# Optimization experiments

Hardware: AMD Instinct MI355X
Metric: run time of the kernel (lower is better)

Reference implementation:

```python
import math
import jax, jax.numpy as jnp
import numpy as np

N_HEAD = 8
BLOCK_SIZE = 1024
LN_EPS = 1e-5


def _layer_norm(x, g, b):
    mu = jnp.mean(x, axis=-1, keepdims=True)
    var = jnp.var(x, axis=-1, keepdims=True)
    return (x - mu) * jax.lax.rsqrt(var + LN_EPS) * g + b


def _skew(QEr):
    # QEr: (B, nh, L, L) -> pad one zero column on the left, reshape, drop first row
    B, nh, nr, nc = QEr.shape
    padded = jnp.pad(QEr, ((0, 0), (0, 0), (0, 0), (1, 0)))  # (B, nh, nr, nc+1)
    reshaped = padded.reshape(B, nh, nc + 1, nr)
    return reshaped[:, :, 1:, :]  # (B, nh, nr, nc)


def _attn(x, W_qkv, b_qkv, W_o, b_o, Er):
    B, L, D = x.shape
    hs = D // N_HEAD
    qkv = x @ W_qkv + b_qkv  # (B, L, 3D)
    q, k, v = jnp.split(qkv, 3, axis=-1)
    # (B, nh, L, hs)
    q = q.reshape(B, L, N_HEAD, hs).transpose(0, 2, 1, 3)
    k = k.reshape(B, L, N_HEAD, hs).transpose(0, 2, 1, 3)
    v = v.reshape(B, L, N_HEAD, hs).transpose(0, 2, 1, 3)
    start = BLOCK_SIZE - L
    Er_t = Er[start:, :].T  # (hs, L)
    QEr = q @ Er_t  # (B, nh, L, L)
    Srel = _skew(QEr)
    scores = (jnp.einsum('bhqd,bhkd->bhqk', q, k) + Srel) * (1.0 / math.sqrt(hs))
    causal = jnp.tril(jnp.ones((L, L), dtype=bool))
    scores = jnp.where(causal, scores, jnp.float32(-jnp.inf))
    att = jax.nn.softmax(scores, axis=-1)
    y = jnp.einsum('bhqk,bhkd->bhqd', att, v)
    y = y.transpose(0, 2, 1, 3).reshape(B, L, D)
    return y @ W_o + b_o


def reference(x, W_qkv, b_qkv, W_o, b_o, Er, ln1_g, ln1_b, ln2_g, ln2_b,
              W_fc, b_fc, W_proj, b_proj):
    x = x + _attn(_layer_norm(x, ln1_g, ln1_b), W_qkv, b_qkv, W_o, b_o, Er)
    h = _layer_norm(x, ln2_g, ln2_b) @ W_fc + b_fc
    h = jax.nn.gelu(h, approximate=False)
    h = h @ W_proj + b_proj
    return x + h


def setup_inputs() -> dict:
    key = jax.random.key(0)
    ks = jax.random.split(key, 8)
    B, L, D, F = 8, 1024, 1024, 4096
    hs = D // N_HEAD
    s = lambda fan_in: 1.0 / math.sqrt(fan_in)
    return {
        'x': jax.random.normal(ks[0], (B, L, D), dtype=jnp.float32),
        'W_qkv': jax.random.normal(ks[1], (D, 3 * D), dtype=jnp.float32) * s(D),
        'b_qkv': jnp.zeros((3 * D,), dtype=jnp.float32),
        'W_o': jax.random.normal(ks[2], (D, D), dtype=jnp.float32) * s(D),
        'b_o': jnp.zeros((D,), dtype=jnp.float32),
        'Er': jax.random.normal(ks[3], (BLOCK_SIZE, hs), dtype=jnp.float32),
        'ln1_g': jnp.ones((D,), dtype=jnp.float32),
        'ln1_b': jnp.zeros((D,), dtype=jnp.float32),
        'ln2_g': jnp.ones((D,), dtype=jnp.float32),
        'ln2_b': jnp.zeros((D,), dtype=jnp.float32),
        'W_fc': jax.random.normal(ks[4], (D, F), dtype=jnp.float32) * s(D),
        'b_fc': jnp.zeros((F,), dtype=jnp.float32),
        'W_proj': jax.random.normal(ks[5], (F, D), dtype=jnp.float32) * s(F),
        'b_proj': jnp.zeros((D,), dtype=jnp.float32),
    }
```

## Files before the change

kernel.cpp:

```cpp
#include <hip/hip_runtime.h>
#include <hip/hip_bf16.h>
#include <math.h>

#define BB 8
#define LL 1024
#define DD 1024
#define FF 4096
#define NHH 8
#define HSS 128
#define SCALE 0.08838834764831845f
#define TRI(qi, kt) ((qi) * ((qi) + 1) / 2 + (kt))

typedef __bf16 bf16;
typedef __bf16 bf16x8 __attribute__((ext_vector_type(8)));
typedef float f32x4 __attribute__((ext_vector_type(4)));
typedef _Float16 f16;
typedef _Float16 f16x4 __attribute__((ext_vector_type(4)));

__device__ inline void async_copy16(const void* g, void* l) {
  __builtin_amdgcn_global_load_lds(
      (const __attribute__((address_space(1))) unsigned int*)g,
      (__attribute__((address_space(3))) unsigned int*)l, 16, 0, 0);
}

#define FENCE() asm volatile("" ::: "memory")
#define BARRIER() do { FENCE(); __builtin_amdgcn_s_barrier(); FENCE(); } while (0)
#define VMCNT0() asm volatile("s_waitcnt vmcnt(0)" ::: "memory")
#define VMCNT2() asm volatile("s_waitcnt vmcnt(2)" ::: "memory")
#define VMCNT4() asm volatile("s_waitcnt vmcnt(4)" ::: "memory")
#define VMCNT6() asm volatile("s_waitcnt vmcnt(6)" ::: "memory")

__global__ __launch_bounds__(256)
void transpose_cast_kernel(const float* __restrict__ W, bf16* __restrict__ Wt,
                           int K, int N) {
  __shared__ float tile[32][33];
  int n0 = blockIdx.x * 32, k0 = blockIdx.y * 32;
  int tx = threadIdx.x, ty = threadIdx.y;
#pragma unroll
  for (int i = 0; i < 32; i += 8)
    tile[ty + i][tx] = W[(size_t)(k0 + ty + i) * N + n0 + tx];
  __syncthreads();
#pragma unroll
  for (int i = 0; i < 32; i += 8)
    Wt[(size_t)(n0 + ty + i) * K + k0 + tx] = (bf16)tile[tx][ty + i];
}

__global__ __launch_bounds__(256)
void pack_er_kernel(const float* __restrict__ Er, bf16* __restrict__ ErP) {
  int g = blockIdx.x, tid = threadIdx.x;
  int l15 = tid & 15, quad = (tid >> 4) & 3, st = tid >> 6;
  const float* src = Er + (size_t)(g * 16 + l15) * HSS + st * 32 + quad * 8;
  bf16* dst = ErP + (size_t)g * 2048 + tid * 8;
#pragma unroll
  for (int j = 0; j < 8; j++) dst[j] = (bf16)src[j];
}

__global__ __launch_bounds__(256)
void ln_kernel(const float* __restrict__ x, const float* __restrict__ g,
               const float* __restrict__ bta, bf16* __restrict__ out) {
  int row = blockIdx.x;
  int tid = threadIdx.x;
  const float4 v = ((const float4*)(x + (size_t)row * DD))[tid];
  float s = v.x + v.y + v.z + v.w;
  float s2 = v.x * v.x + v.y * v.y + v.z * v.z + v.w * v.w;
#pragma unroll
  for (int o = 32; o > 0; o >>= 1) {
    s += __shfl_down(s, o);
    s2 += __shfl_down(s2, o);
  }
  __shared__ float a1[4], a2[4];
  int wave = tid >> 6;
  if ((tid & 63) == 0) { a1[wave] = s; a2[wave] = s2; }
  __syncthreads();
  s = a1[0] + a1[1] + a1[2] + a1[3];
  s2 = a2[0] + a2[1] + a2[2] + a2[3];
  float mu = s * (1.0f / DD);
  float rstd = rsqrtf(s2 * (1.0f / DD) - mu * mu + 1e-5f);
  float4 gv = ((const float4*)g)[tid];
  float4 bv = ((const float4*)bta)[tid];
  bf16* o4 = out + (size_t)row * DD + tid * 4;
  o4[0] = (bf16)((v.x - mu) * rstd * gv.x + bv.x);
  o4[1] = (bf16)((v.y - mu) * rstd * gv.y + bv.y);
  o4[2] = (bf16)((v.z - mu) * rstd * gv.z + bv.z);
  o4[3] = (bf16)((v.w - mu) * rstd * gv.w + bv.w);
}

template <int EPI>
__global__ __launch_bounds__(512)
void gemm256_kernel(const bf16* __restrict__ A, const bf16* __restrict__ Bt,
                    const float* __restrict__ bias, void* __restrict__ Cout,
                    int M, int N, int K) {
  __shared__ bf16 Als[2][256 * 64];
  __shared__ bf16 Bls[2][256 * 64];
  int tid = threadIdx.x;
  int wave = tid >> 6, lane = tid & 63;
  int l15 = lane & 15, quad = lane >> 4;
  int wmi = wave >> 2, wni = wave & 3;
  int m0 = blockIdx.y * 256, n0 = blockIdx.x * 256;

  int u0 = tid, u1 = tid + 512;
  int r0 = u0 >> 3, c0 = ((u0 & 7) ^ (r0 & 7)) << 3;
  int r1 = u1 >> 3, c1 = ((u1 & 7) ^ (r1 & 7)) << 3;
  const bf16* aB0 = A + (size_t)(m0 + r0) * K + c0;
  const bf16* aB1 = A + (size_t)(m0 + r1) * K + c1;
  const bf16* bB0 = Bt + (size_t)(n0 + r0) * K + c0;
  const bf16* bB1 = Bt + (size_t)(n0 + r1) * K + c1;
  int d0 = u0 * 8, d1 = u1 * 8;

  auto stageA = [&](int b, int h, int t) {
    size_t off = (size_t)h * 128 * K + (size_t)t * 64;
    async_copy16(aB0 + off, &Als[b][h * 8192 + d0]);
    async_copy16(aB1 + off, &Als[b][h * 8192 + d1]);
  };
  auto stageB = [&](int b, int h, int t) {
    size_t off = (size_t)h * 128 * K + (size_t)t * 64;
    async_copy16(bB0 + off, &Bls[b][h * 8192 + d0]);
    async_copy16(bB1 + off, &Bls[b][h * 8192 + d1]);
  };

  f32x4 acc[8][4] = {};
  bf16x8 af[2][4], bfr[2][2][2];

  auto readA = [&](int b, int qm) {
#pragma unroll
    for (int kk = 0; kk < 2; kk++)
#pragma unroll
      for (int mt = 0; mt < 4; mt++) {
        int ra = qm * 128 + wmi * 64 + mt * 16 + l15;
        af[kk][mt] = *(const bf16x8*)&Als[b][ra * 64 + (((kk * 4 + quad) ^ (ra & 7)) << 3)];
      }
  };
  auto readB = [&](int b, int qn) {
#pragma unroll
    for (int kk = 0; kk < 2; kk++)
#pragma unroll
      for (int nt = 0; nt < 2; nt++) {
        int rb = qn * 128 + wni * 32 + nt * 16 + l15;
        bfr[qn][kk][nt] = *(const bf16x8*)&Bls[b][rb * 64 + (((kk * 4 + quad) ^ (rb & 7)) << 3)];
      }
  };
  auto mfma16 = [&](int qm, int qn) {
    __builtin_amdgcn_s_setprio(1);
#pragma unroll
    for (int kk = 0; kk < 2; kk++)
#pragma unroll
      for (int mt = 0; mt < 4; mt++)
#pragma unroll
        for (int nt = 0; nt < 2; nt++)
          acc[qm * 4 + mt][qn * 2 + nt] = __builtin_amdgcn_mfma_f32_16x16x32_bf16(
              af[kk][mt], bfr[qn][kk][nt], acc[qm * 4 + mt][qn * 2 + nt], 0, 0, 0);
    __builtin_amdgcn_s_setprio(0);
  };

  int nk = K >> 6;
  stageA(0, 0, 0); stageB(0, 0, 0); stageB(0, 1, 0); stageA(0, 1, 0);
  stageA(1, 0, 1); stageB(1, 1, 1);
  VMCNT6();
  BARRIER();

  for (int t = 0; t < nk; t += 2) {
#pragma unroll
    for (int uu = 0; uu < 2; uu++) {
      const int tt = t + uu;
      const int cur = uu;
      readA(cur, 0); readB(cur, 0); readB(cur, 1);
      if (tt + 1 < nk) stageB(cur ^ 1, 0, tt + 1);
      BARRIER();
      mfma16(0, 0);
      BARRIER();
      if (tt + 1 < nk) stageA(cur ^ 1, 1, tt + 1);
      VMCNT6();
      BARRIER();
      mfma16(0, 1);
      BARRIER();
      readA(cur, 1);
      if (tt + 2 < nk) stageA(cur, 0, tt + 2);
      BARRIER();
      mfma16(1, 1);
      BARRIER();
      if (tt + 2 < nk) stageB(cur, 1, tt + 2);
      VMCNT6();
      BARRIER();
      mfma16(1, 0);
      BARRIER();
    }
  }

#pragma unroll
  for (int MT = 0; MT < 8; MT++) {
#pragma unroll
    for (int NT = 0; NT < 4; NT++) {
      int col = n0 + (NT >> 1) * 128 + wni * 32 + (NT & 1) * 16 + l15;
      float bv = bias[col];
#pragma unroll
      for (int r = 0; r < 4; r++) {
        int row = m0 + (MT >> 2) * 128 + wmi * 64 + (MT & 3) * 16 + quad * 4 + r;
        float v = acc[MT][NT][r] + bv;
        if (EPI == 1) v = 0.5f * v * (1.0f + erff(v * 0.7071067811865475f));
        ((bf16*)Cout)[(size_t)row * N + col] = (bf16)v;
      }
    }
  }
}

template <int EPI>
__global__ __launch_bounds__(512)
void gemm256n_kernel(const bf16* __restrict__ A, const bf16* __restrict__ Bt,
                     const float* __restrict__ bias, const float* __restrict__ res,
                     void* __restrict__ Cout, int M, int N, int K) {
  __shared__ bf16 Als[2][256 * 64];
  __shared__ bf16 Bls[2][128 * 64];
  int tid = threadIdx.x;
  int wave = tid >> 6, lane = tid & 63;
  int l15 = lane & 15, quad = lane >> 4;
  int wmi = wave >> 2, wni = wave & 3;
  int m0 = blockIdx.y * 256, n0 = blockIdx.x * 128;

  int u0 = tid, u1 = tid + 512;
  int r0 = u0 >> 3, c0 = ((u0 & 7) ^ (r0 & 7)) << 3;
  int r1 = u1 >> 3, c1 = ((u1 & 7) ^ (r1 & 7)) << 3;
  const bf16* aB0 = A + (size_t)(m0 + r0) * K + c0;
  const bf16* aB1 = A + (size_t)(m0 + r1) * K + c1;
  const bf16* bB0 = Bt + (size_t)(n0 + r0) * K + c0;
  const bf16* bB1 = Bt + (size_t)(n0 + r1) * K + c1;
  int d0 = u0 * 8, d1 = u1 * 8;

  auto stageA = [&](int b, int h, int t) {
    size_t off = (size_t)h * 128 * K + (size_t)t * 64;
    async_copy16(aB0 + off, &Als[b][h * 8192 + d0]);
    async_copy16(aB1 + off, &Als[b][h * 8192 + d1]);
  };
  auto stageB = [&](int b, int t) {
    size_t off = (size_t)t * 64;
    async_copy16(bB0 + off, &Bls[b][d0]);
    async_copy16(bB1 + off, &Bls[b][d1]);
  };

  f32x4 acc[8][2] = {};
  bf16x8 af[2][4], bfr[2][2];

  auto readA = [&](int b, int qm) {
#pragma unroll
    for (int kk = 0; kk < 2; kk++)
#pragma unroll
      for (int mt = 0; mt < 4; mt++) {
        int ra = qm * 128 + wmi * 64 + mt * 16 + l15;
        af[kk][mt] = *(const bf16x8*)&Als[b][ra * 64 + (((kk * 4 + quad) ^ (ra & 7)) << 3)];
      }
  };
  auto readB = [&](int b) {
#pragma unroll
    for (int kk = 0; kk < 2; kk++)
#pragma unroll
      for (int nt = 0; nt < 2; nt++) {
        int rb = wni * 32 + nt * 16 + l15;
        bfr[kk][nt] = *(const bf16x8*)&Bls[b][rb * 64 + (((kk * 4 + quad) ^ (rb & 7)) << 3)];
      }
  };
  auto mfma16 = [&](int qm) {
    __builtin_amdgcn_s_setprio(1);
#pragma unroll
    for (int kk = 0; kk < 2; kk++)
#pragma unroll
      for (int mt = 0; mt < 4; mt++)
#pragma unroll
        for (int nt = 0; nt < 2; nt++)
          acc[qm * 4 + mt][nt] = __builtin_amdgcn_mfma_f32_16x16x32_bf16(
              af[kk][mt], bfr[kk][nt], acc[qm * 4 + mt][nt], 0, 0, 0);
    __builtin_amdgcn_s_setprio(0);
  };

  int nk = K >> 6;
  stageB(0, 0); stageB(1, 1); stageA(0, 0, 0); stageA(0, 1, 0);
  VMCNT0();
  BARRIER();

  for (int t = 0; t < nk; t += 2) {
#pragma unroll
    for (int uu = 0; uu < 2; uu++) {
      const int tt = t + uu;
      const int cur = uu;
      readA(cur, 0); readB(cur);
      if (tt + 1 < nk) { stageA(cur ^ 1, 0, tt + 1); VMCNT4(); }
      else { VMCNT0(); }
      BARRIER();
      mfma16(0);
      BARRIER();
      readA(cur, 1);
      if (tt + 1 < nk) stageA(cur ^ 1, 1, tt + 1);
      if (tt + 2 < nk) { stageB(cur, tt + 2); VMCNT4(); }
      else { VMCNT2(); }
      BARRIER();
      mfma16(1);
      BARRIER();
    }
  }

#pragma unroll
  for (int MT = 0; MT < 8; MT++) {
#pragma unroll
    for (int NT = 0; NT < 2; NT++) {
      int col = n0 + wni * 32 + NT * 16 + l15;
      float bv = bias[col];
#pragma unroll
      for (int r = 0; r < 4; r++) {
        int row = m0 + (MT >> 2) * 128 + wmi * 64 + (MT & 3) * 16 + quad * 4 + r;
        float v = acc[MT][NT][r] + bv;
        if (EPI == 2) {
          v += res[(size_t)row * N + col];
          ((float*)Cout)[(size_t)row * N + col] = v;
        } else {
          ((bf16*)Cout)[(size_t)row * N + col] = (bf16)v;
        }
      }
    }
  }
}

template <int EPI>
__global__ __launch_bounds__(256)
void gemm_kernel(const bf16* __restrict__ A, const bf16* __restrict__ Bt,
                 const float* __restrict__ bias, const float* __restrict__ res,
                 void* __restrict__ Cout, int M, int N, int K) {
  __shared__ bf16 Als[128 * 64];
  __shared__ bf16 Bls[128 * 64];
  int tid = threadIdx.x;
  int wave = tid >> 6, lane = tid & 63;
  int l15 = lane & 15, quad = lane >> 4;

  int m0 = blockIdx.y * 128, n0 = blockIdx.x * 128;
  int wm = (wave >> 1) * 64, wn = (wave & 1) * 64;
  f32x4 acc[4][4] = {};

  const bf16* asrc[4];
  const bf16* bsrc[4];
  int ldso[4];
#pragma unroll
  for (int i = 0; i < 4; i++) {
    int u = i * 256 + tid;
    int row = u >> 3, c = u & 7;
    int g = c ^ (row & 7);
    asrc[i] = A + (size_t)(m0 + row) * K + g * 8;
    bsrc[i] = Bt + (size_t)(n0 + row) * K + g * 8;
    ldso[i] = u * 8;
  }

  for (int k0 = 0; k0 < K; k0 += 64) {
    __syncthreads();
#pragma unroll
    for (int i = 0; i < 4; i++) {
      async_copy16(asrc[i] + k0, &Als[ldso[i]]);
      async_copy16(bsrc[i] + k0, &Bls[ldso[i]]);
    }
    __syncthreads();

    bf16x8 af[2][4], bfr[2][4];
#pragma unroll
    for (int kk = 0; kk < 2; kk++) {
#pragma unroll
      for (int mt = 0; mt < 4; mt++) {
        int ra = wm + mt * 16 + l15;
        af[kk][mt] = *(const bf16x8*)&Als[ra * 64 + (((kk * 4 + quad) ^ (ra & 7)) << 3)];
        int rb = wn + mt * 16 + l15;
        bfr[kk][mt] = *(const bf16x8*)&Bls[rb * 64 + (((kk * 4 + quad) ^ (rb & 7)) << 3)];
      }
    }
#pragma unroll
    for (int kk = 0; kk < 2; kk++)
#pragma unroll
      for (int mt = 0; mt < 4; mt++)
#pragma unroll
        for (int nt = 0; nt < 4; nt++)
          acc[mt][nt] = __builtin_amdgcn_mfma_f32_16x16x32_bf16(af[kk][mt], bfr[kk][nt],
                                                                acc[mt][nt], 0, 0, 0);
  }

#pragma unroll
  for (int mt = 0; mt < 4; mt++) {
#pragma unroll
    for (int nt = 0; nt < 4; nt++) {
      int col = n0 + wn + nt * 16 + l15;
      float bv = bias[col];
#pragma unroll
      for (int r = 0; r < 4; r++) {
        int row = m0 + wm + mt * 16 + quad * 4 + r;
        float v = acc[mt][nt][r] + bv;
        if (EPI == 1) v = 0.5f * v * (1.0f + erff(v * 0.7071067811865475f));
        if (EPI == 2) {
          v += res[(size_t)row * N + col];
          ((float*)Cout)[(size_t)row * N + col] = v;
        } else {
          ((bf16*)Cout)[(size_t)row * N + col] = (bf16)v;
        }
      }
    }
  }
}

__global__ __launch_bounds__(256)
void pack_kv_kernel(const bf16* __restrict__ qkv, bf16* __restrict__ Kpack,
                    bf16* __restrict__ Vpack) {
  __shared__ bf16 Vst[64][132];
  int kt = blockIdx.x, h = blockIdx.y, b = blockIdx.z;
  int tid = threadIdx.x;
  const size_t rs = 3 * DD;
  const bf16* kb = qkv + (size_t)b * LL * rs + (size_t)(kt * 64) * rs + DD + h * HSS;
  const bf16* vb = kb + DD;
  bf16* kp = Kpack + ((size_t)(b * NHH + h) * 16 + kt) * (64 * 128);
  bf16* vp = Vpack + ((size_t)(b * NHH + h) * 16 + kt) * (128 * 64);
#pragma unroll
  for (int i = 0; i < 4; i++) {
    int u = i * 256 + tid;
    int kk = u >> 4, c = u & 15;
    bf16x8 kv = *(const bf16x8*)(kb + (size_t)kk * rs + c * 8);
    *(bf16x8*)(kp + kk * 128 + ((c ^ kk) & 15) * 8) = kv;
    *(bf16x8*)&Vst[kk][c * 8] = *(const bf16x8*)(vb + (size_t)kk * rs + c * 8);
  }
  __syncthreads();
#pragma unroll
  for (int i = 0; i < 4; i++) {
    int u = i * 256 + tid;
    int d = u >> 3, c = u & 7;
    bf16x8 t;
#pragma unroll
    for (int j = 0; j < 8; j++) t[j] = Vst[c * 8 + j][d];
    *(bf16x8*)(vp + d * 64 + ((c ^ (d & 7))) * 8) = t;
  }
}

__global__ __launch_bounds__(256)
void relband_kernel(const bf16* __restrict__ qkv, const bf16* __restrict__ ErP,
                    f16* __restrict__ band) {
  int tid = threadIdx.x, wave = tid >> 6, lane = tid & 63;
  int l15 = lane & 15, quad = lane >> 4;
  int h = blockIdx.y, b = blockIdx.z;
  const size_t rs = 3 * DD;
  const bf16* qbase = qkv + (size_t)b * LL * rs + h * HSS;
  f16* bbase = band + (size_t)(b * NHH + h) * (136 * 4096);

#pragma unroll 1
  for (int ph = 0; ph < 2; ph++) {
    int qb = ph ? 15 - blockIdx.x : blockIdx.x;
    int qw0 = qb * 64 + wave * 16;

    bf16x8 qf[4];
#pragma unroll
    for (int st = 0; st < 4; st++)
      qf[st] = *(const bf16x8*)(qbase + (size_t)(qw0 + l15) * rs + st * 32 + quad * 8);

#pragma unroll 1
    for (int kt = 0; kt <= qb; kt++) {
      int k0 = kt * 64;
      int kmax_off = qw0 + 15 - k0;
      int m_base = 1008 - qw0 + k0;
      int gb = m_base >> 4;
      int ntR = (kmax_off >> 4) + 1;
      if (ntR > 4) ntR = 4;

      f32x4 rr[5] = {};
#pragma unroll
      for (int n = 0; n < 5; n++) {
        if (n <= ntR) {
          int g = gb + n;
          if (g > 63) g = 63;
          const bf16* ep = ErP + (size_t)g * 2048 + lane * 8;
#pragma unroll
          for (int st = 0; st < 4; st++) {
            bf16x8 ef = *(const bf16x8*)(ep + st * 512);
            rr[n] = __builtin_amdgcn_mfma_f32_16x16x32_bf16(qf[st], ef, rr[n], 0, 0, 0);
          }
        }
      }

      f16x4 sf[4];
#pragma unroll
      for (int rg = 0; rg < 4; rg++) {
        int qloc = quad * 4 + rg;
        int tt = 15 - qloc + l15;
        int src = (lane & 48) | (tt & 15);
        float shv[5];
#pragma unroll
        for (int n = 0; n < 5; n++)
          shv[n] = (n <= ntR) ? __shfl(rr[n][rg], src) : 0.f;
#pragma unroll
        for (int nt = 0; nt < 4; nt++)
          sf[nt][rg] = (f16)((tt & 16) ? shv[nt + 1] : shv[nt]);
      }
      f16* tb = bbase + (size_t)TRI(qb, kt) * 4096;
#pragma unroll
      for (int nt = 0; nt < 4; nt++)
        if (nt * 16 <= kmax_off)
          *(f16x4*)(tb + (wave * 4 + nt) * 256 + l15 * 16 + quad * 4) = sf[nt];
    }
  }
}

__global__ __launch_bounds__(256)
void flash_kernel(const bf16* __restrict__ qkv, const bf16* __restrict__ Kpack,
                  const bf16* __restrict__ Vpack, const f16* __restrict__ band,
                  bf16* __restrict__ y) {
  __shared__ bf16 Kls[2][64 * 128];
  __shared__ bf16 Vls[2][128 * 64];
  __shared__ bf16 Pls[4][16][72];

  int tid = threadIdx.x, wave = tid >> 6, lane = tid & 63;
  int l15 = lane & 15, quad = lane >> 4;
  int h = blockIdx.y, b = blockIdx.z;

  const size_t rs = 3 * DD;
  const bf16* qbase = qkv + (size_t)b * LL * rs + h * HSS;
  const bf16* kp = Kpack + (size_t)(b * NHH + h) * 16 * (64 * 128);
  const bf16* vp = Vpack + (size_t)(b * NHH + h) * 16 * (128 * 64);
  const f16* bnd = band + (size_t)(b * NHH + h) * (136 * 4096);

  int buf = 0;
#pragma unroll 1
  for (int ph = 0; ph < 2; ph++) {
    int qb = ph ? 15 - blockIdx.x : blockIdx.x;
    int qw0 = qb * 64 + wave * 16;
    int nkt = qb + 1;

    bf16x8 qf[4];
#pragma unroll
    for (int st = 0; st < 4; st++)
      qf[st] = *(const bf16x8*)(qbase + (size_t)(qw0 + l15) * rs + st * 32 + quad * 8);

    {
      const bf16* ks = kp;
      const bf16* vs = vp;
#pragma unroll
      for (int i = 0; i < 4; i++) {
        int off = (wave * 4 + i) * 512 + lane * 8;
        async_copy16(ks + off, &Kls[buf][off]);
        async_copy16(vs + off, &Vls[buf][off]);
      }
    }

    f32x4 o[8] = {};
    float mrow[4] = {-INFINITY, -INFINITY, -INFINITY, -INFINITY};
    float lrow[4] = {0.f, 0.f, 0.f, 0.f};

#pragma unroll 1
    for (int kt = 0; kt < nkt; kt++) {
      int k0 = kt * 64;
      int kmax_off = qw0 + 15 - k0;
      __syncthreads();

      const f16* tb = bnd + (size_t)TRI(qb, kt) * 4096;
      f16x4 srl[4] = {};
#pragma unroll
      for (int nt = 0; nt < 4; nt++)
        if (nt * 16 <= kmax_off)
          srl[nt] = *(const f16x4*)(tb + (wave * 4 + nt) * 256 + l15 * 16 + quad * 4);

      if (kt + 1 < nkt) {
        const bf16* ks = kp + (size_t)(kt + 1) * (64 * 128);
        const bf16* vs = vp + (size_t)(kt + 1) * (128 * 64);
#pragma unroll
        for (int i = 0; i < 4; i++) {
          int off = (wave * 4 + i) * 512 + lane * 8;
          async_copy16(ks + off, &Kls[buf ^ 1][off]);
          async_copy16(vs + off, &Vls[buf ^ 1][off]);
        }
      }

      f32x4 sa[4] = {};
#pragma unroll
      for (int nt = 0; nt < 4; nt++) {
        if (nt * 16 <= kmax_off) {
          int kk = nt * 16 + l15;
#pragma unroll
          for (int st = 0; st < 4; st++) {
            bf16x8 kf = *(const bf16x8*)&Kls[buf][kk * 128 + (((st * 4 + quad) ^ l15) & 15) * 8];
            sa[nt] = __builtin_amdgcn_mfma_f32_16x16x32_bf16(qf[st], kf, sa[nt], 0, 0, 0);
          }
        }
      }

      float pmx[4] = {-INFINITY, -INFINITY, -INFINITY, -INFINITY};
#pragma unroll
      for (int nt = 0; nt < 4; nt++) {
        if (nt * 16 <= kmax_off) {
          int kg = k0 + nt * 16 + l15;
#pragma unroll
          for (int rg = 0; rg < 4; rg++) {
            int qg = qw0 + quad * 4 + rg;
            float v = (sa[nt][rg] + (float)srl[nt][rg]) * SCALE;
            v = (kg <= qg) ? v : -INFINITY;
            sa[nt][rg] = v;
            pmx[rg] = fmaxf(pmx[rg], v);
          }
        } else {
#pragma unroll
          for (int rg = 0; rg < 4; rg++) sa[nt][rg] = -INFINITY;
        }
      }

#pragma unroll
      for (int rg = 0; rg < 4; rg++) {
        float v = pmx[rg];
        v = fmaxf(v, __shfl_xor(v, 1));
        v = fmaxf(v, __shfl_xor(v, 2));
        v = fmaxf(v, __shfl_xor(v, 4));
        v = fmaxf(v, __shfl_xor(v, 8));
        float mnew = fmaxf(mrow[rg], v);
        float alpha = __expf(mrow[rg] - mnew);
        mrow[rg] = mnew;
        lrow[rg] *= alpha;
#pragma unroll
        for (int nt = 0; nt < 8; nt++) o[nt][rg] *= alpha;
        pmx[rg] = mnew;
      }
      float ls[4] = {0.f, 0.f, 0.f, 0.f};
#pragma unroll
      for (int nt = 0; nt < 4; nt++)
#pragma unroll
        for (int rg = 0; rg < 4; rg++) {
          float p = __expf(sa[nt][rg] - pmx[rg]);
          ls[rg] += p;
          Pls[wave][quad * 4 + rg][nt * 16 + l15] = (bf16)p;
        }
#pragma unroll
      for (int rg = 0; rg < 4; rg++) {
        float v = ls[rg];
        v += __shfl_xor(v, 1);
        v += __shfl_xor(v, 2);
        v += __shfl_xor(v, 4);
        v += __shfl_xor(v, 8);
        lrow[rg] += v;
      }

      bf16x8 pf[2];
#pragma unroll
      for (int s2 = 0; s2 < 2; s2++)
        pf[s2] = *(const bf16x8*)&Pls[wave][l15][s2 * 32 + quad * 8];
#pragma unroll
      for (int nt = 0; nt < 8; nt++) {
        int d = nt * 16 + l15;
#pragma unroll
        for (int s2 = 0; s2 < 2; s2++) {
          if (s2 * 32 <= kmax_off) {
            bf16x8 vf = *(const bf16x8*)&Vls[buf][d * 64 + (((s2 * 4 + quad) ^ (l15 & 7)) & 7) * 8];
            o[nt] = __builtin_amdgcn_mfma_f32_16x16x32_bf16(pf[s2], vf, o[nt], 0, 0, 0);
          }
        }
      }
      buf ^= 1;
    }

#pragma unroll
    for (int rg = 0; rg < 4; rg++) {
      float inv = 1.0f / lrow[rg];
      int qg = qw0 + quad * 4 + rg;
      bf16* yr = y + ((size_t)b * LL + qg) * DD + h * HSS;
#pragma unroll
      for (int nt = 0; nt < 8; nt++) yr[nt * 16 + l15] = (bf16)(o[nt][rg] * inv);
    }
  }
}

extern "C" void kernel_launch(void* const* d_in, const int* in_sizes, int n_in,
                              void* d_out, int out_size, void* d_ws, size_t ws_size,
                              hipStream_t stream) {
  const float* x = (const float*)d_in[0];
  const float* W_qkv = (const float*)d_in[1];
  const float* b_qkv = (const float*)d_in[2];
  const float* W_o = (const float*)d_in[3];
  const float* b_o = (const float*)d_in[4];
  const float* Er = (const float*)d_in[5];
  const float* ln1_g = (const float*)d_in[6];
  const float* ln1_b = (const float*)d_in[7];
  const float* ln2_g = (const float*)d_in[8];
  const float* ln2_b = (const float*)d_in[9];
  const float* W_fc = (const float*)d_in[10];
  const float* b_fc = (const float*)d_in[11];
  const float* W_proj = (const float*)d_in[12];
  const float* b_proj = (const float*)d_in[13];
  float* out = (float*)d_out;

  char* p = (char*)d_ws;
  auto alloc = [&](size_t bytes) {
    char* r = p;
    p += (bytes + 255) & ~(size_t)255;
    return r;
  };
  bf16* Wt_qkv = (bf16*)alloc((size_t)3072 * 1024 * 2);
  bf16* Wt_o   = (bf16*)alloc((size_t)1024 * 1024 * 2);
  bf16* Wt_fc  = (bf16*)alloc((size_t)4096 * 1024 * 2);
  bf16* Wt_pr  = (bf16*)alloc((size_t)1024 * 4096 * 2);
  bf16* ErP    = (bf16*)alloc((size_t)1024 * 128 * 2);
  bf16* xn     = (bf16*)alloc((size_t)8192 * 1024 * 2);
  bf16* qkvb   = (bf16*)alloc((size_t)8192 * 3072 * 2);
  bf16* yb     = (bf16*)alloc((size_t)8192 * 1024 * 2);
  bf16* Kpack  = (bf16*)alloc((size_t)64 * 16 * 64 * 128 * 2);
  bf16* Vpack  = (bf16*)alloc((size_t)64 * 16 * 128 * 64 * 2);
  f16*  band   = (f16*)alloc((size_t)64 * 136 * 4096 * 2);
  float* x2    = (float*)band;
  bf16* hb     = qkvb;

  transpose_cast_kernel<<<dim3(3072 / 32, 1024 / 32), dim3(32, 8), 0, stream>>>(W_qkv, Wt_qkv, 1024, 3072);
  transpose_cast_kernel<<<dim3(1024 / 32, 1024 / 32), dim3(32, 8), 0, stream>>>(W_o, Wt_o, 1024, 1024);
  transpose_cast_kernel<<<dim3(4096 / 32, 1024 / 32), dim3(32, 8), 0, stream>>>(W_fc, Wt_fc, 1024, 4096);
  transpose_cast_kernel<<<dim3(1024 / 32, 4096 / 32), dim3(32, 8), 0, stream>>>(W_proj, Wt_pr, 4096, 1024);
  pack_er_kernel<<<64, 256, 0, stream>>>(Er, ErP);

  ln_kernel<<<8192, 256, 0, stream>>>(x, ln1_g, ln1_b, xn);
  gemm256n_kernel<0><<<dim3(24, 32), 512, 0, stream>>>(xn, Wt_qkv, b_qkv, nullptr, qkvb, 8192, 3072, 1024);
  pack_kv_kernel<<<dim3(16, 8, 8), 256, 0, stream>>>(qkvb, Kpack, Vpack);
  relband_kernel<<<dim3(8, 8, 8), 256, 0, stream>>>(qkvb, ErP, band);
  flash_kernel<<<dim3(8, 8, 8), 256, 0, stream>>>(qkvb, Kpack, Vpack, band, yb);
  gemm_kernel<2><<<dim3(8, 64), 256, 0, stream>>>(yb, Wt_o, b_o, x, x2, 8192, 1024, 1024);
  ln_kernel<<<8192, 256, 0, stream>>>(x2, ln2_g, ln2_b, xn);
  gemm256_kernel<1><<<dim3(16, 32), 512, 0, stream>>>(xn, Wt_fc, b_fc, hb, 8192, 4096, 1024);
  gemm256n_kernel<2><<<dim3(8, 32), 512, 0, stream>>>(hb, Wt_pr, b_proj, x2, out, 8192, 1024, 4096);
}
```

Baseline: 591.8 us.

## Fuse weight prep launches, load K directly in flash, lazy softmax rescale, setprio

Merges the four weight transpose-casts and the Er pack into one prep launch. Drops the separate K packing: the flash kernel now async-loads K straight from the qkv buffer with a swizzled layout, and pack_kv becomes V-only. The online softmax skips rescaling unless the running max rises by more than a threshold, and MFMA sections are wrapped in s_setprio. The output projection moves from the 128-tile gemm to the 256-tile gemm256n kernel. The price is strided K loads from global memory and a lazy-max softmax that depends on the threshold staying numerically safe in fp32.

Result: slower. 604.6 us (+2.2%).

```diff
diff --git a/kernel.cpp b/kernel.cpp
--- a/kernel.cpp
+++ b/kernel.cpp
@@ -31,11 +31,31 @@
 #define VMCNT6() asm volatile("s_waitcnt vmcnt(6)" ::: "memory")
 
 __global__ __launch_bounds__(256)
-void transpose_cast_kernel(const float* __restrict__ W, bf16* __restrict__ Wt,
-                           int K, int N) {
+void prep_kernel(const float* __restrict__ Wq, const float* __restrict__ Wo,
+                 const float* __restrict__ Wf, const float* __restrict__ Wp,
+                 const float* __restrict__ Er, bf16* __restrict__ Wtq,
+                 bf16* __restrict__ Wto, bf16* __restrict__ Wtf,
+                 bf16* __restrict__ Wtp, bf16* __restrict__ ErP) {
   __shared__ float tile[32][33];
-  int n0 = blockIdx.x * 32, k0 = blockIdx.y * 32;
-  int tx = threadIdx.x, ty = threadIdx.y;
+  int id = blockIdx.x, tid = threadIdx.x;
+  if (id >= 12288) {
+    int g = id - 12288;
+    int l15 = tid & 15, quad = (tid >> 4) & 3, st = tid >> 6;
+    const float* src = Er + (size_t)(g * 16 + l15) * HSS + st * 32 + quad * 8;
+    bf16* dst = ErP + (size_t)g * 2048 + tid * 8;
+#pragma unroll
+    for (int j = 0; j < 8; j++) dst[j] = (bf16)src[j];
+    return;
+  }
+  const float* W;
+  bf16* Wt;
+  int K, N, bx, by;
+  if (id < 3072)      { W = Wq; Wt = Wtq; K = 1024; N = 3072; bx = id % 96;  by = id / 96; }
+  else if (id < 4096) { id -= 3072; W = Wo; Wt = Wto; K = 1024; N = 1024; bx = id % 32;  by = id / 32; }
+  else if (id < 8192) { id -= 4096; W = Wf; Wt = Wtf; K = 1024; N = 4096; bx = id % 128; by = id / 128; }
+  else                { id -= 8192; W = Wp; Wt = Wtp; K = 4096; N = 1024; bx = id % 32;  by = id / 32; }
+  int n0 = bx * 32, k0 = by * 32;
+  int tx = tid & 31, ty = tid >> 5;
 #pragma unroll
   for (int i = 0; i < 32; i += 8)
     tile[ty + i][tx] = W[(size_t)(k0 + ty + i) * N + n0 + tx];
@@ -43,16 +63,6 @@
 #pragma unroll
   for (int i = 0; i < 32; i += 8)
     Wt[(size_t)(n0 + ty + i) * K + k0 + tx] = (bf16)tile[tx][ty + i];
-}
-
-__global__ __launch_bounds__(256)
-void pack_er_kernel(const float* __restrict__ Er, bf16* __restrict__ ErP) {
-  int g = blockIdx.x, tid = threadIdx.x;
-  int l15 = tid & 15, quad = (tid >> 4) & 3, st = tid >> 6;
-  const float* src = Er + (size_t)(g * 16 + l15) * HSS + st * 32 + quad * 8;
-  bf16* dst = ErP + (size_t)g * 2048 + tid * 8;
-#pragma unroll
-  for (int j = 0; j < 8; j++) dst[j] = (bf16)src[j];
 }
 
 __global__ __launch_bounds__(256)
@@ -306,85 +316,6 @@
       for (int r = 0; r < 4; r++) {
         int row = m0 + (MT >> 2) * 128 + wmi * 64 + (MT & 3) * 16 + quad * 4 + r;
         float v = acc[MT][NT][r] + bv;
-        if (EPI == 2) {
-          v += res[(size_t)row * N + col];
-          ((float*)Cout)[(size_t)row * N + col] = v;
-        } else {
-          ((bf16*)Cout)[(size_t)row * N + col] = (bf16)v;
-        }
-      }
-    }
-  }
-}
-
-template <int EPI>
-__global__ __launch_bounds__(256)
-void gemm_kernel(const bf16* __restrict__ A, const bf16* __restrict__ Bt,
-                 const float* __restrict__ bias, const float* __restrict__ res,
-                 void* __restrict__ Cout, int M, int N, int K) {
-  __shared__ bf16 Als[128 * 64];
-  __shared__ bf16 Bls[128 * 64];
-  int tid = threadIdx.x;
-  int wave = tid >> 6, lane = tid & 63;
-  int l15 = lane & 15, quad = lane >> 4;
-
-  int m0 = blockIdx.y * 128, n0 = blockIdx.x * 128;
-  int wm = (wave >> 1) * 64, wn = (wave & 1) * 64;
-  f32x4 acc[4][4] = {};
-
-  const bf16* asrc[4];
-  const bf16* bsrc[4];
-  int ldso[4];
-#pragma unroll
-  for (int i = 0; i < 4; i++) {
-    int u = i * 256 + tid;
-    int row = u >> 3, c = u & 7;
-    int g = c ^ (row & 7);
-    asrc[i] = A + (size_t)(m0 + row) * K + g * 8;
-    bsrc[i] = Bt + (size_t)(n0 + row) * K + g * 8;
-    ldso[i] = u * 8;
-  }
-
-  for (int k0 = 0; k0 < K; k0 += 64) {
-    __syncthreads();
-#pragma unroll
-    for (int i = 0; i < 4; i++) {
-      async_copy16(asrc[i] + k0, &Als[ldso[i]]);
-      async_copy16(bsrc[i] + k0, &Bls[ldso[i]]);
-    }
-    __syncthreads();
-
-    bf16x8 af[2][4], bfr[2][4];
-#pragma unroll
-    for (int kk = 0; kk < 2; kk++) {
-#pragma unroll
-      for (int mt = 0; mt < 4; mt++) {
-        int ra = wm + mt * 16 + l15;
-        af[kk][mt] = *(const bf16x8*)&Als[ra * 64 + (((kk * 4 + quad) ^ (ra & 7)) << 3)];
-        int rb = wn + mt * 16 + l15;
-        bfr[kk][mt] = *(const bf16x8*)&Bls[rb * 64 + (((kk * 4 + quad) ^ (rb & 7)) << 3)];
-      }
-    }
-#pragma unroll
-    for (int kk = 0; kk < 2; kk++)
-#pragma unroll
-      for (int mt = 0; mt < 4; mt++)
-#pragma unroll
-        for (int nt = 0; nt < 4; nt++)
-          acc[mt][nt] = __builtin_amdgcn_mfma_f32_16x16x32_bf16(af[kk][mt], bfr[kk][nt],
-                                                                acc[mt][nt], 0, 0, 0);
-  }
-
-#pragma unroll
-  for (int mt = 0; mt < 4; mt++) {
-#pragma unroll
-    for (int nt = 0; nt < 4; nt++) {
-      int col = n0 + wn + nt * 16 + l15;
-      float bv = bias[col];
-#pragma unroll
-      for (int r = 0; r < 4; r++) {
-        int row = m0 + wm + mt * 16 + quad * 4 + r;
-        float v = acc[mt][nt][r] + bv;
         if (EPI == 1) v = 0.5f * v * (1.0f + erff(v * 0.7071067811865475f));
         if (EPI == 2) {
           v += res[(size_t)row * N + col];
@@ -398,22 +329,17 @@
 }
 
 __global__ __launch_bounds__(256)
-void pack_kv_kernel(const bf16* __restrict__ qkv, bf16* __restrict__ Kpack,
-                    bf16* __restrict__ Vpack) {
+void pack_v_kernel(const bf16* __restrict__ qkv, bf16* __restrict__ Vpack) {
   __shared__ bf16 Vst[64][132];
   int kt = blockIdx.x, h = blockIdx.y, b = blockIdx.z;
   int tid = threadIdx.x;
   const size_t rs = 3 * DD;
-  const bf16* kb = qkv + (size_t)b * LL * rs + (size_t)(kt * 64) * rs + DD + h * HSS;
-  const bf16* vb = kb + DD;
-  bf16* kp = Kpack + ((size_t)(b * NHH + h) * 16 + kt) * (64 * 128);
+  const bf16* vb = qkv + (size_t)b * LL * rs + (size_t)(kt * 64) * rs + 2 * DD + h * HSS;
   bf16* vp = Vpack + ((size_t)(b * NHH + h) * 16 + kt) * (128 * 64);
 #pragma unroll
   for (int i = 0; i < 4; i++) {
     int u = i * 256 + tid;
     int kk = u >> 4, c = u & 15;
-    bf16x8 kv = *(const bf16x8*)(kb + (size_t)kk * rs + c * 8);
-    *(bf16x8*)(kp + kk * 128 + ((c ^ kk) & 15) * 8) = kv;
     *(bf16x8*)&Vst[kk][c * 8] = *(const bf16x8*)(vb + (size_t)kk * rs + c * 8);
   }
   __syncthreads();
@@ -458,6 +384,7 @@
       if (ntR > 4) ntR = 4;
 
       f32x4 rr[5] = {};
+      __builtin_amdgcn_s_setprio(1);
 #pragma unroll
       for (int n = 0; n < 5; n++) {
         if (n <= ntR) {
@@ -471,6 +398,7 @@
           }
         }
       }
+      __builtin_amdgcn_s_setprio(0);
 
       f16x4 sf[4];
 #pragma unroll
@@ -496,9 +424,8 @@
 }
 
 __global__ __launch_bounds__(256)
-void flash_kernel(const bf16* __restrict__ qkv, const bf16* __restrict__ Kpack,
-                  const bf16* __restrict__ Vpack, const f16* __restrict__ band,
-                  bf16* __restrict__ y) {
+void flash_kernel(const bf16* __restrict__ qkv, const bf16* __restrict__ Vpack,
+                  const f16* __restrict__ band, bf16* __restrict__ y) {
   __shared__ bf16 Kls[2][64 * 128];
   __shared__ bf16 Vls[2][128 * 64];
   __shared__ bf16 Pls[4][16][72];
@@ -509,9 +436,20 @@
 
   const size_t rs = 3 * DD;
   const bf16* qbase = qkv + (size_t)b * LL * rs + h * HSS;
-  const bf16* kp = Kpack + (size_t)(b * NHH + h) * 16 * (64 * 128);
+  const bf16* kb = qbase + DD;
   const bf16* vp = Vpack + (size_t)(b * NHH + h) * 16 * (128 * 64);
   const f16* bnd = band + (size_t)(b * NHH + h) * (136 * 4096);
+
+  size_t koff[4];
+  int ldso[4];
+#pragma unroll
+  for (int i = 0; i < 4; i++) {
+    int off = (wave * 4 + i) * 512 + lane * 8;
+    int u = off >> 3;
+    int kk = u >> 4, c = u & 15;
+    koff[i] = (size_t)kk * rs + (size_t)(((c ^ kk) & 15) * 8);
+    ldso[i] = off;
+  }
 
   int buf = 0;
 #pragma unroll 1
@@ -525,15 +463,10 @@
     for (int st = 0; st < 4; st++)
       qf[st] = *(const bf16x8*)(qbase + (size_t)(qw0 + l15) * rs + st * 32 + quad * 8);
 
-    {
-      const bf16* ks = kp;
-      const bf16* vs = vp;
-#pragma unroll
-      for (int i = 0; i < 4; i++) {
-        int off = (wave * 4 + i) * 512 + lane * 8;
-        async_copy16(ks + off, &Kls[buf][off]);
-        async_copy16(vs + off, &Vls[buf][off]);
-      }
+#pragma unroll
+    for (int i = 0; i < 4; i++) {
+      async_copy16(kb + koff[i], &Kls[buf][ldso[i]]);
+      async_copy16(vp + ldso[i], &Vls[buf][ldso[i]]);
     }
 
     f32x4 o[8] = {};
@@ -554,17 +487,17 @@
           srl[nt] = *(const f16x4*)(tb + (wave * 4 + nt) * 256 + l15 * 16 + quad * 4);
 
       if (kt + 1 < nkt) {
-        const bf16* ks = kp + (size_t)(kt + 1) * (64 * 128);
+        const bf16* ks = kb + (size_t)(kt + 1) * 64 * rs;
         const bf16* vs = vp + (size_t)(kt + 1) * (128 * 64);
 #pragma unroll
         for (int i = 0; i < 4; i++) {
-          int off = (wave * 4 + i) * 512 + lane * 8;
-          async_copy16(ks + off, &Kls[buf ^ 1][off]);
-          async_copy16(vs + off, &Vls[buf ^ 1][off]);
+          async_copy16(ks + koff[i], &Kls[buf ^ 1][ldso[i]]);
+          async_copy16(vs + ldso[i], &Vls[buf ^ 1][ldso[i]]);
         }
       }
 
       f32x4 sa[4] = {};
+      __builtin_amdgcn_s_setprio(1);
 #pragma unroll
       for (int nt = 0; nt < 4; nt++) {
         if (nt * 16 <= kmax_off) {
@@ -576,6 +509,7 @@
           }
         }
       }
+      __builtin_amdgcn_s_setprio(0);
 
       float pmx[4] = {-INFINITY, -INFINITY, -INFINITY, -INFINITY};
 #pragma unroll
@@ -596,6 +530,8 @@
         }
       }
 
+      float vmx[4];
+      bool need = false;
 #pragma unroll
       for (int rg = 0; rg < 4; rg++) {
         float v = pmx[rg];
@@ -603,14 +539,23 @@
         v = fmaxf(v, __shfl_xor(v, 2));
         v = fmaxf(v, __shfl_xor(v, 4));
         v = fmaxf(v, __shfl_xor(v, 8));
-        float mnew = fmaxf(mrow[rg], v);
-        float alpha = __expf(mrow[rg] - mnew);
-        mrow[rg] = mnew;
-        lrow[rg] *= alpha;
-#pragma unroll
-        for (int nt = 0; nt < 8; nt++) o[nt][rg] *= alpha;
-        pmx[rg] = mnew;
-      }
+        vmx[rg] = v;
+        need = need || (v - mrow[rg] > 8.0f);
+      }
+      if (__any(need)) {
+#pragma unroll
+        for (int rg = 0; rg < 4; rg++) {
+          float mnew = fmaxf(mrow[rg], vmx[rg]);
+          float alpha = __expf(mrow[rg] - mnew);
+          mrow[rg] = mnew;
+          lrow[rg] *= alpha;
+#pragma unroll
+          for (int nt = 0; nt < 8; nt++) o[nt][rg] *= alpha;
+        }
+      }
+#pragma unroll
+      for (int rg = 0; rg < 4; rg++) pmx[rg] = mrow[rg];
+
       float ls[4] = {0.f, 0.f, 0.f, 0.f};
 #pragma unroll
       for (int nt = 0; nt < 4; nt++)
@@ -634,6 +579,7 @@
 #pragma unroll
       for (int s2 = 0; s2 < 2; s2++)
         pf[s2] = *(const bf16x8*)&Pls[wave][l15][s2 * 32 + quad * 8];
+      __builtin_amdgcn_s_setprio(1);
 #pragma unroll
       for (int nt = 0; nt < 8; nt++) {
         int d = nt * 16 + l15;
@@ -645,6 +591,7 @@
           }
         }
       }
+      __builtin_amdgcn_s_setprio(0);
       buf ^= 1;
     }
 
@@ -692,24 +639,20 @@
   bf16* xn     = (bf16*)alloc((size_t)8192 * 1024 * 2);
   bf16* qkvb   = (bf16*)alloc((size_t)8192 * 3072 * 2);
   bf16* yb     = (bf16*)alloc((size_t)8192 * 1024 * 2);
-  bf16* Kpack  = (bf16*)alloc((size_t)64 * 16 * 64 * 128 * 2);
   bf16* Vpack  = (bf16*)alloc((size_t)64 * 16 * 128 * 64 * 2);
   f16*  band   = (f16*)alloc((size_t)64 * 136 * 4096 * 2);
   float* x2    = (float*)band;
   bf16* hb     = qkvb;
 
-  transpose_cast_kernel<<<dim3(3072 / 32, 1024 / 32), dim3(32, 8), 0, stream>>>(W_qkv, Wt_qkv, 1024, 3072);
-  transpose_cast_kernel<<<dim3(1024 / 32, 1024 / 32), dim3(32, 8), 0, stream>>>(W_o, Wt_o, 1024, 1024);
-  transpose_cast_kernel<<<dim3(4096 / 32, 1024 / 32), dim3(32, 8), 0, stream>>>(W_fc, Wt_fc, 1024, 4096);
-  transpose_cast_kernel<<<dim3(1024 / 32, 4096 / 32), dim3(32, 8), 0, stream>>>(W_proj, Wt_pr, 4096, 1024);
-  pack_er_kernel<<<64, 256, 0, stream>>>(Er, ErP);
+  prep_kernel<<<12352, 256, 0, stream>>>(W_qkv, W_o, W_fc, W_proj, Er,
+                                         Wt_qkv, Wt_o, Wt_fc, Wt_pr, ErP);
 
   ln_kernel<<<8192, 256, 0, stream>>>(x, ln1_g, ln1_b, xn);
   gemm256n_kernel<0><<<dim3(24, 32), 512, 0, stream>>>(xn, Wt_qkv, b_qkv, nullptr, qkvb, 8192, 3072, 1024);
-  pack_kv_kernel<<<dim3(16, 8, 8), 256, 0, stream>>>(qkvb, Kpack, Vpack);
+  pack_v_kernel<<<dim3(16, 8, 8), 256, 0, stream>>>(qkvb, Vpack);
   relband_kernel<<<dim3(8, 8, 8), 256, 0, stream>>>(qkvb, ErP, band);
-  flash_kernel<<<dim3(8, 8, 8), 256, 0, stream>>>(qkvb, Kpack, Vpack, band, yb);
-  gemm_kernel<2><<<dim3(8, 64), 256, 0, stream>>>(yb, Wt_o, b_o, x, x2, 8192, 1024, 1024);
+  flash_kernel<<<dim3(8, 8, 8), 256, 0, stream>>>(qkvb, Vpack, band, yb);
+  gemm256n_kernel<2><<<dim3(8, 32), 512, 0, stream>>>(yb, Wt_o, b_o, x, x2, 8192, 1024, 1024);
   ln_kernel<<<8192, 256, 0, stream>>>(x2, ln2_g, ln2_b, xn);
   gemm256_kernel<1><<<dim3(16, 32), 512, 0, stream>>>(xn, Wt_fc, b_fc, hb, 8192, 4096, 1024);
   gemm256n_kernel<2><<<dim3(8, 32), 512, 0, stream>>>(hb, Wt_pr, b_proj, x2, out, 8192, 1024, 4096);
```
